# Performance work log

Hardware: AMD Instinct MI355X
Metric: run time of the kernel (lower is better)

The kernel has to match this reference:

```python
import jax, jax.numpy as jnp
import numpy as np

B, V, F, H, W = 8, 5023, 9976, 512, 512
L = 5  # lights


def setup_inputs() -> dict:
    key = jax.random.key(0)
    ks = jax.random.split(key, 7)
    return {
        "vertices": jax.random.normal(ks[0], (B, V, 3), jnp.float32),
        "transformed_vertices": jax.random.normal(ks[1], (B, V, 3), jnp.float32),
        "lights": jax.random.normal(ks[2], (B, L, 6), jnp.float32),
        "images": jax.random.uniform(ks[3], (B, 3, H, W), jnp.float32),
        "bary": jax.random.uniform(ks[4], (B, H, W, 3), jnp.float32) + 1e-3,
        "faces": jax.random.randint(ks[5], (F, 3), 0, V),
        "pix_to_face": jax.random.randint(ks[6], (B, H, W), 0, F + 1),  # ==F -> background
    }


def _face_vertices(verts, faces):
    # verts [B,V,3], faces [F,3] -> [B,F,3,3]  (gather)
    return verts[:, faces]


def _vertex_normals(verts, faces):
    # gather face verts, per-face cross products, scatter-add back to vertices
    fv = verts[:, faces]                       # [B,F,3,3]
    v0, v1, v2 = fv[:, :, 0], fv[:, :, 1], fv[:, :, 2]
    n = jnp.zeros_like(verts)
    n = n.at[:, faces[:, 1]].add(jnp.cross(v2 - v1, v0 - v1))
    n = n.at[:, faces[:, 2]].add(jnp.cross(v0 - v2, v1 - v2))
    n = n.at[:, faces[:, 0]].add(jnp.cross(v1 - v0, v2 - v0))
    return n / jnp.maximum(jnp.linalg.norm(n, axis=-1, keepdims=True), 1e-6)


def _add_directionlight(normals, lights):
    # normals [B,N,3], lights [B,L,6] -> shading [B,N,3]
    d = lights[:, :, :3]
    d = d / jnp.maximum(jnp.linalg.norm(d, axis=-1, keepdims=True), 1e-12)
    ndl = jnp.clip(jnp.einsum("bnc,blc->bln", normals, d), 0.0, 1.0)  # [B,L,N]
    return jnp.mean(ndl[..., None] * lights[:, :, None, 3:], axis=1)


def reference(vertices, transformed_vertices, lights, images, bary, faces, pix_to_face):
    sg = jax.lax.stop_gradient
    b, nv, _ = vertices.shape
    nf = faces.shape[0]
    h, w = pix_to_face.shape[1], pix_to_face.shape[2]

    tv = transformed_vertices.at[:, :, 2].add(10.0)

    fverts = _face_vertices(vertices, faces)                 # [B,F,3,3]
    normals = _vertex_normals(vertices, faces)               # [B,V,3]
    fnorm = _face_vertices(normals, faces)                   # [B,F,3,3]
    tnorm = _vertex_normals(tv, faces)
    tfnorm = _face_vertices(tnorm, faces)

    colors = jnp.full((b, nf, 3, 3), 180.0 / 255.0, vertices.dtype)  # face_colors buffer
    uv = jnp.zeros((b, nf, 3, 3), vertices.dtype)                    # face_uvcoords (unused downstream)
    # attribute channels: [0:3]=albedo [3:6]=tfnorm [6:9]=verts [9:12]=fnorm [12:15]=uv
    attrs = jnp.concatenate([colors, sg(tfnorm), sg(fverts), fnorm, uv], axis=-1)  # [B,F,3,15]

    # --- rasterizer interpolation stage ---
    p2f = pix_to_face.reshape(b, -1)                         # [B,HW]
    valid = (p2f < nf).astype(vertices.dtype)[..., None]     # [B,HW,1] alpha channel
    fidx = jnp.minimum(p2f, nf - 1)
    pa = jax.vmap(lambda a, i: a[i])(attrs, fidx)            # [B,HW,3,15]
    bw = bary.reshape(b, -1, 3)
    bw = bw / jnp.sum(bw, axis=-1, keepdims=True)
    interp = jnp.einsum("bpk,bpkc->bpc", bw, pa)             # [B,HW,15]

    albedo = interp[..., 0:3]
    tnormal_map = sg(interp[..., 3:6])
    pos_mask = (tnormal_map[..., 2:3] < 0.15).astype(vertices.dtype)
    normal_images = sg(interp[..., 9:12])
    alpha = sg(valid) * pos_mask                             # [B,HW,1]

    shading = _add_directionlight(normal_images, lights)     # [B,HW,3]
    shaded = albedo * shading

    imgs = images.transpose(0, 2, 3, 1).reshape(b, -1, 3)
    out = shaded * alpha + imgs * (1.0 - alpha)              # [B,HW,3]
    return out.reshape(b, h, w, 3).transpose(0, 3, 1, 2)     # [B,3,H,W]
```

## Files before the change

### kernel.cpp

```cpp
#include <hip/hip_runtime.h>
#include <stdint.h>

namespace {

constexpr int kB = 8;
constexpr int kV = 5023;
constexpr int kF = 9976;
constexpr int kH = 512;
constexpr int kW = 512;
constexpr int kL = 5;
constexpr int kHW = kH * kW;
constexpr int kQ = kHW / 4;
constexpr int kQH = kQ / 2;
constexpr int kCap = 32;

typedef float nfloat4 __attribute__((ext_vector_type(4)));

__device__ __forceinline__ float h2f(uint32_t u) {
  _Float16 h;
  uint16_t s = (uint16_t)u;
  __builtin_memcpy(&h, &s, 2);
  return (float)h;
}
__device__ __forceinline__ uint32_t f2h(float f) {
  _Float16 h = (_Float16)f;
  uint16_t s;
  __builtin_memcpy(&s, &h, 2);
  return (uint32_t)s;
}

__device__ __forceinline__ void cross3(float ax, float ay, float az,
                                       float bx, float by, float bz,
                                       float& cx, float& cy, float& cz) {
  cx = ay * bz - az * by;
  cy = az * bx - ax * bz;
  cz = ax * by - ay * bx;
}

__global__ void init_kernel(int* __restrict__ cnt,
                            const float* __restrict__ lights,
                            float4* __restrict__ ldir4) {
  int idx = blockIdx.x * blockDim.x + threadIdx.x;
  for (int i = idx; i < kV; i += gridDim.x * blockDim.x) cnt[i] = 0;
  if (idx < kB * kL) {
    float dx = lights[idx * 6 + 0];
    float dy = lights[idx * 6 + 1];
    float dz = lights[idx * 6 + 2];
    float inv = 1.0f / fmaxf(sqrtf(dx * dx + dy * dy + dz * dz), 1e-12f);
    ldir4[idx * 2 + 0] = make_float4(dx * inv, dy * inv, dz * inv, 0.0f);
    ldir4[idx * 2 + 1] =
        make_float4(lights[idx * 6 + 3], lights[idx * 6 + 4], lights[idx * 6 + 5], 0.0f);
  }
}

__global__ void prep_kernel(const float* __restrict__ verts,
                            const float* __restrict__ tverts,
                            const int* __restrict__ faces,
                            int* __restrict__ cnt,
                            int* __restrict__ adj,
                            float4* __restrict__ fn) {
  int idx = blockIdx.x * blockDim.x + threadIdx.x;
  if (idx < kF) {
    int f = idx;
#pragma unroll
    for (int c = 0; c < 3; ++c) {
      int v = faces[f * 3 + c];
      int slot = atomicAdd(&cnt[v], 1);
      if (slot < kCap) adj[v * kCap + slot] = f;
    }
    return;
  }
  idx -= kF;
  if (idx >= kB * kF) return;
  int b = idx / kF;
  int f = idx - b * kF;
  int i0 = faces[f * 3 + 0];
  int i1 = faces[f * 3 + 1];
  int i2 = faces[f * 3 + 2];

  float nx, ny, nz, tx, ty, tz;
  {
    const float* vb = verts + (size_t)b * kV * 3;
    float v0x = vb[i0 * 3 + 0], v0y = vb[i0 * 3 + 1], v0z = vb[i0 * 3 + 2];
    float v1x = vb[i1 * 3 + 0], v1y = vb[i1 * 3 + 1], v1z = vb[i1 * 3 + 2];
    float v2x = vb[i2 * 3 + 0], v2y = vb[i2 * 3 + 1], v2z = vb[i2 * 3 + 2];
    cross3(v1x - v0x, v1y - v0y, v1z - v0z, v2x - v0x, v2y - v0y, v2z - v0z,
           nx, ny, nz);
  }
  {
    const float* vb = tverts + (size_t)b * kV * 3;
    float v0x = vb[i0 * 3 + 0], v0y = vb[i0 * 3 + 1], v0z = vb[i0 * 3 + 2] + 10.0f;
    float v1x = vb[i1 * 3 + 0], v1y = vb[i1 * 3 + 1], v1z = vb[i1 * 3 + 2] + 10.0f;
    float v2x = vb[i2 * 3 + 0], v2y = vb[i2 * 3 + 1], v2z = vb[i2 * 3 + 2] + 10.0f;
    cross3(v1x - v0x, v1y - v0y, v1z - v0z, v2x - v0x, v2y - v0y, v2z - v0z,
           tx, ty, tz);
  }
  fn[(size_t)idx * 2 + 0] = make_float4(nx, ny, nz, tx);
  fn[(size_t)idx * 2 + 1] = make_float4(ty, tz, 0.0f, 0.0f);
}

__global__ void gather_normalize_kernel(const int* __restrict__ cnt,
                                        const int* __restrict__ adj,
                                        const float4* __restrict__ fn,
                                        uint4* __restrict__ vrec) {
  int idx = blockIdx.x * blockDim.x + threadIdx.x;
  if (idx >= kB * kV) return;
  int b = idx / kV;
  int v = idx - b * kV;
  int e = min(cnt[v], kCap);
  float nx = 0.f, ny = 0.f, nz = 0.f, tx = 0.f, ty = 0.f, tzv = 0.f;
  const int* av = adj + v * kCap;
  for (int j = 0; j < e; ++j) {
    int f = av[j];
    size_t k = ((size_t)b * kF + f) * 2;
    float4 a = fn[k];
    float4 c = fn[k + 1];
    nx += a.x;
    ny += a.y;
    nz += a.z;
    tx += a.w;
    ty += c.x;
    tzv += c.y;
  }
  float inv = 1.0f / fmaxf(sqrtf(nx * nx + ny * ny + nz * nz), 1e-6f);
  float invt = 1.0f / fmaxf(sqrtf(tx * tx + ty * ty + tzv * tzv), 1e-6f);
  uint4 r;
  r.x = f2h(nx * inv) | (f2h(ny * inv) << 16);
  r.y = f2h(nz * inv);
  r.z = __float_as_uint(tzv * invt);
  r.w = 0;
  vrec[idx] = r;
}

__global__ void faceattr_kernel(const int* __restrict__ faces,
                                const uint4* __restrict__ vrec,
                                uint4* __restrict__ fattr) {
  int b = blockIdx.x % kB;
  int f = (blockIdx.x / kB) * blockDim.x + threadIdx.x;
  if (f >= kF) return;
  int idx = b * kF + f;
  int i0 = faces[f * 3 + 0];
  int i1 = faces[f * 3 + 1];
  int i2 = faces[f * 3 + 2];
  const uint4* vb = vrec + (size_t)b * kV;
  uint4 r0 = vb[i0];
  uint4 r1 = vb[i1];
  uint4 r2 = vb[i2];
  uint4 w0, w1;
  w0.x = r0.x;
  w0.y = (r0.y & 0xffffu) | (r1.x << 16);
  w0.z = (r1.x >> 16) | ((r1.y & 0xffffu) << 16);
  w0.w = r2.x;
  w1.x = r2.y & 0xffffu;
  w1.y = r0.z;
  w1.z = r1.z;
  w1.w = r2.z;
  fattr[(size_t)idx * 2 + 0] = w0;
  fattr[(size_t)idx * 2 + 1] = w1;
}

__device__ __forceinline__ void shade_quad(
    const int4& f4, const float4& w0, const float4& w1, const float4& w2,
    const uint4* A, const uint4* T,
    const float4& im0, const float4& im1, const float4& im2,
    const float4* lb4, float o[3][4]) {
  int fi[4] = {f4.x, f4.y, f4.z, f4.w};
  float bw[4][3] = {{w0.x, w0.y, w0.z},
                    {w0.w, w1.x, w1.y},
                    {w1.z, w1.w, w2.x},
                    {w2.y, w2.z, w2.w}};
  float im[3][4] = {{im0.x, im0.y, im0.z, im0.w},
                    {im1.x, im1.y, im1.z, im1.w},
                    {im2.x, im2.y, im2.z, im2.w}};
#pragma unroll
  for (int k = 0; k < 4; ++k) {
    float b0 = bw[k][0], b1 = bw[k][1], b2 = bw[k][2];
    float inv = 1.0f / (b0 + b1 + b2);
    b0 *= inv;
    b1 *= inv;
    b2 *= inv;
    float n0x = h2f(A[k].x), n0y = h2f(A[k].x >> 16);
    float n0z = h2f(A[k].y), n1x = h2f(A[k].y >> 16);
    float n1y = h2f(A[k].z), n1z = h2f(A[k].z >> 16);
    float n2x = h2f(A[k].w), n2y = h2f(A[k].w >> 16);
    float n2z = h2f(T[k].x);
    float tz0 = __uint_as_float(T[k].y);
    float tz1 = __uint_as_float(T[k].z);
    float tz2 = __uint_as_float(T[k].w);

    float tzi = b0 * tz0 + b1 * tz1 + b2 * tz2;
    bool alpha = (fi[k] < kF) && (tzi < 0.15f);
    float nx = b0 * n0x + b1 * n1x + b2 * n2x;
    float ny = b0 * n0y + b1 * n1y + b2 * n2y;
    float nz = b0 * n0z + b1 * n1z + b2 * n2z;
    float s0 = 0.f, s1 = 0.f, s2 = 0.f;
#pragma unroll
    for (int l = 0; l < kL; ++l) {
      float4 d4 = lb4[l * 2 + 0];
      float4 c4 = lb4[l * 2 + 1];
      float d = nx * d4.x + ny * d4.y + nz * d4.z;
      d = fminf(fmaxf(d, 0.0f), 1.0f);
      s0 += d * c4.x;
      s1 += d * c4.y;
      s2 += d * c4.z;
    }
    const float kk = (180.0f / 255.0f) / (float)kL;
    o[0][k] = alpha ? kk * s0 : im[0][k];
    o[1][k] = alpha ? kk * s1 : im[1][k];
    o[2][k] = alpha ? kk * s2 : im[2][k];
  }
}

__global__ void __launch_bounds__(256) pixel8_kernel(
    const int4* __restrict__ p2f4,
    const float4* __restrict__ bary4,
    const uint4* __restrict__ fattr,
    const float4* __restrict__ ldir4,
    const float4* __restrict__ img4,
    float4* __restrict__ out4) {
  int b = blockIdx.x & 7;
  int q0 = (blockIdx.x >> 3) * blockDim.x + threadIdx.x;
  int q1 = q0 + kQH;
  size_t gA = (size_t)b * kQ + q0;
  size_t gB = (size_t)b * kQ + q1;

  int4 fA = p2f4[gA];
  int4 fB = p2f4[gB];
  float4 wA0 = bary4[gA * 3 + 0];
  float4 wA1 = bary4[gA * 3 + 1];
  float4 wA2 = bary4[gA * 3 + 2];
  float4 wB0 = bary4[gB * 3 + 0];
  float4 wB1 = bary4[gB * 3 + 1];
  float4 wB2 = bary4[gB * 3 + 2];

  size_t ibA = (size_t)b * 3 * kQ + q0;
  size_t ibB = (size_t)b * 3 * kQ + q1;
  float4 iA0 = img4[ibA + 0 * (size_t)kQ];
  float4 iA1 = img4[ibA + 1 * (size_t)kQ];
  float4 iA2 = img4[ibA + 2 * (size_t)kQ];
  float4 iB0 = img4[ibB + 0 * (size_t)kQ];
  float4 iB1 = img4[ibB + 1 * (size_t)kQ];
  float4 iB2 = img4[ibB + 2 * (size_t)kQ];

  uint4 AA[4], TA[4], AB[4], TB[4];
  {
    int fiA[4] = {fA.x, fA.y, fA.z, fA.w};
    int fiB[4] = {fB.x, fB.y, fB.z, fB.w};
#pragma unroll
    for (int k = 0; k < 4; ++k) {
      int f = (fiA[k] < kF) ? fiA[k] : (kF - 1);
      size_t base = ((size_t)b * kF + f) * 2;
      AA[k] = fattr[base + 0];
      TA[k] = fattr[base + 1];
    }
#pragma unroll
    for (int k = 0; k < 4; ++k) {
      int f = (fiB[k] < kF) ? fiB[k] : (kF - 1);
      size_t base = ((size_t)b * kF + f) * 2;
      AB[k] = fattr[base + 0];
      TB[k] = fattr[base + 1];
    }
  }

  int bu = __builtin_amdgcn_readfirstlane(b);
  const float4* lb4 = ldir4 + (size_t)bu * kL * 2;

  float oA[3][4];
  shade_quad(fA, wA0, wA1, wA2, AA, TA, iA0, iA1, iA2, lb4, oA);
#pragma unroll
  for (int c = 0; c < 3; ++c) {
    nfloat4 v = {oA[c][0], oA[c][1], oA[c][2], oA[c][3]};
    __builtin_nontemporal_store(v, (nfloat4*)&out4[ibA + c * (size_t)kQ]);
  }

  float oB[3][4];
  shade_quad(fB, wB0, wB1, wB2, AB, TB, iB0, iB1, iB2, lb4, oB);
#pragma unroll
  for (int c = 0; c < 3; ++c) {
    nfloat4 v = {oB[c][0], oB[c][1], oB[c][2], oB[c][3]};
    __builtin_nontemporal_store(v, (nfloat4*)&out4[ibB + c * (size_t)kQ]);
  }
}

}

extern "C" void kernel_launch(void* const* d_in, const int* in_sizes, int n_in,
                              void* d_out, int out_size, void* d_ws, size_t ws_size,
                              hipStream_t stream) {
  const float* vertices = (const float*)d_in[0];
  const float* tvertices = (const float*)d_in[1];
  const float* lights = (const float*)d_in[2];
  const float* images = (const float*)d_in[3];
  const float* bary = (const float*)d_in[4];
  const int* faces = (const int*)d_in[5];
  const int* p2f = (const int*)d_in[6];
  float* out = (float*)d_out;

  char* ws = (char*)d_ws;
  int* cnt = (int*)ws;
  ws += ((size_t)kV * sizeof(int) + 15) & ~15ull;
  int* adj = (int*)ws;
  ws += ((size_t)kV * kCap * sizeof(int) + 15) & ~15ull;
  float4* fn = (float4*)ws;
  ws += (size_t)kB * kF * 2 * sizeof(float4);
  uint4* vrec = (uint4*)ws;
  ws += (size_t)kB * kV * sizeof(uint4);
  float4* ldir4 = (float4*)ws;
  ws += (size_t)kB * kL * 2 * sizeof(float4);
  uint4* fattr = (uint4*)ws;

  {
    init_kernel<<<20, 256, 0, stream>>>(cnt, lights, ldir4);
  }
  {
    int n = kF + kB * kF;
    prep_kernel<<<(n + 255) / 256, 256, 0, stream>>>(vertices, tvertices, faces, cnt,
                                                     adj, fn);
  }
  {
    int n = kB * kV;
    gather_normalize_kernel<<<(n + 255) / 256, 256, 0, stream>>>(cnt, adj, fn, vrec);
  }
  {
    int chunks = (kF + 255) / 256;
    faceattr_kernel<<<chunks * kB, 256, 0, stream>>>(faces, vrec, fattr);
  }
  {
    pixel8_kernel<<<(kQH / 256) * kB, 256, 0, stream>>>(
        (const int4*)p2f, (const float4*)bary, fattr, ldir4, (const float4*)images,
        (float4*)out);
  }
}
```

Measured before the change: 47.02 us.

## Fuse four preprocessing kernels into one cooperative kernel with grid syncs

Merges the init, per-face normal, vertex gather-normalize and face-attribute kernels into one cooperative launch, with grid.sync() between the phases. The goal is to remove three kernel launches and their inter-kernel gaps. The grid is about 351 blocks of 256 threads, which must all be co-resident for a cooperative launch, and each grid-wide sync adds its own cost. Phase work is mapped directly by thread index, so every phase fits within this one grid.

Measured after the change: 161.6 us. 244% more time.

```diff
diff --git a/kernel.cpp b/kernel.cpp
--- a/kernel.cpp
+++ b/kernel.cpp
@@ -1,5 +1,8 @@
 #include <hip/hip_runtime.h>
+#include <hip/hip_cooperative_groups.h>
 #include <stdint.h>
+
+namespace cg = cooperative_groups;
 
 namespace {
 
@@ -14,6 +17,9 @@
 constexpr int kQH = kQ / 2;
 constexpr int kCap = 32;
 
+constexpr int kCoopThreads = kF + kB * kF;
+constexpr int kCoopBlocks = (kCoopThreads + 255) / 256;
+
 typedef float nfloat4 __attribute__((ext_vector_type(4)));
 
 __device__ __forceinline__ float h2f(uint32_t u) {
@@ -37,11 +43,21 @@
   cz = ax * by - ay * bx;
 }
 
-__global__ void init_kernel(int* __restrict__ cnt,
-                            const float* __restrict__ lights,
-                            float4* __restrict__ ldir4) {
-  int idx = blockIdx.x * blockDim.x + threadIdx.x;
-  for (int i = idx; i < kV; i += gridDim.x * blockDim.x) cnt[i] = 0;
+__global__ void fused_prep_kernel(const float* __restrict__ verts,
+                                  const float* __restrict__ tverts,
+                                  const int* __restrict__ faces,
+                                  const float* __restrict__ lights,
+                                  int* __restrict__ cnt,
+                                  int* __restrict__ adj,
+                                  float4* __restrict__ fn,
+                                  uint4* __restrict__ vrec,
+                                  uint4* __restrict__ fattr,
+                                  float4* __restrict__ ldir4) {
+  cg::grid_group grid = cg::this_grid();
+  const int idx = blockIdx.x * blockDim.x + threadIdx.x;
+  const int nthr = gridDim.x * blockDim.x;
+
+  for (int i = idx; i < kV; i += nthr) cnt[i] = 0;
   if (idx < kB * kL) {
     float dx = lights[idx * 6 + 0];
     float dy = lights[idx * 6 + 1];
@@ -51,15 +67,8 @@
     ldir4[idx * 2 + 1] =
         make_float4(lights[idx * 6 + 3], lights[idx * 6 + 4], lights[idx * 6 + 5], 0.0f);
   }
-}
-
-__global__ void prep_kernel(const float* __restrict__ verts,
-                            const float* __restrict__ tverts,
-                            const int* __restrict__ faces,
-                            int* __restrict__ cnt,
-                            int* __restrict__ adj,
-                            float4* __restrict__ fn) {
-  int idx = blockIdx.x * blockDim.x + threadIdx.x;
+  grid.sync();
+
   if (idx < kF) {
     int f = idx;
 #pragma unroll
@@ -68,95 +77,86 @@
       int slot = atomicAdd(&cnt[v], 1);
       if (slot < kCap) adj[v * kCap + slot] = f;
     }
-    return;
-  }
-  idx -= kF;
-  if (idx >= kB * kF) return;
-  int b = idx / kF;
-  int f = idx - b * kF;
-  int i0 = faces[f * 3 + 0];
-  int i1 = faces[f * 3 + 1];
-  int i2 = faces[f * 3 + 2];
-
-  float nx, ny, nz, tx, ty, tz;
-  {
-    const float* vb = verts + (size_t)b * kV * 3;
-    float v0x = vb[i0 * 3 + 0], v0y = vb[i0 * 3 + 1], v0z = vb[i0 * 3 + 2];
-    float v1x = vb[i1 * 3 + 0], v1y = vb[i1 * 3 + 1], v1z = vb[i1 * 3 + 2];
-    float v2x = vb[i2 * 3 + 0], v2y = vb[i2 * 3 + 1], v2z = vb[i2 * 3 + 2];
-    cross3(v1x - v0x, v1y - v0y, v1z - v0z, v2x - v0x, v2y - v0y, v2z - v0z,
-           nx, ny, nz);
-  }
-  {
-    const float* vb = tverts + (size_t)b * kV * 3;
-    float v0x = vb[i0 * 3 + 0], v0y = vb[i0 * 3 + 1], v0z = vb[i0 * 3 + 2] + 10.0f;
-    float v1x = vb[i1 * 3 + 0], v1y = vb[i1 * 3 + 1], v1z = vb[i1 * 3 + 2] + 10.0f;
-    float v2x = vb[i2 * 3 + 0], v2y = vb[i2 * 3 + 1], v2z = vb[i2 * 3 + 2] + 10.0f;
-    cross3(v1x - v0x, v1y - v0y, v1z - v0z, v2x - v0x, v2y - v0y, v2z - v0z,
-           tx, ty, tz);
-  }
-  fn[(size_t)idx * 2 + 0] = make_float4(nx, ny, nz, tx);
-  fn[(size_t)idx * 2 + 1] = make_float4(ty, tz, 0.0f, 0.0f);
-}
-
-__global__ void gather_normalize_kernel(const int* __restrict__ cnt,
-                                        const int* __restrict__ adj,
-                                        const float4* __restrict__ fn,
-                                        uint4* __restrict__ vrec) {
-  int idx = blockIdx.x * blockDim.x + threadIdx.x;
-  if (idx >= kB * kV) return;
-  int b = idx / kV;
-  int v = idx - b * kV;
-  int e = min(cnt[v], kCap);
-  float nx = 0.f, ny = 0.f, nz = 0.f, tx = 0.f, ty = 0.f, tzv = 0.f;
-  const int* av = adj + v * kCap;
-  for (int j = 0; j < e; ++j) {
-    int f = av[j];
-    size_t k = ((size_t)b * kF + f) * 2;
-    float4 a = fn[k];
-    float4 c = fn[k + 1];
-    nx += a.x;
-    ny += a.y;
-    nz += a.z;
-    tx += a.w;
-    ty += c.x;
-    tzv += c.y;
-  }
-  float inv = 1.0f / fmaxf(sqrtf(nx * nx + ny * ny + nz * nz), 1e-6f);
-  float invt = 1.0f / fmaxf(sqrtf(tx * tx + ty * ty + tzv * tzv), 1e-6f);
-  uint4 r;
-  r.x = f2h(nx * inv) | (f2h(ny * inv) << 16);
-  r.y = f2h(nz * inv);
-  r.z = __float_as_uint(tzv * invt);
-  r.w = 0;
-  vrec[idx] = r;
-}
-
-__global__ void faceattr_kernel(const int* __restrict__ faces,
-                                const uint4* __restrict__ vrec,
-                                uint4* __restrict__ fattr) {
-  int b = blockIdx.x % kB;
-  int f = (blockIdx.x / kB) * blockDim.x + threadIdx.x;
-  if (f >= kF) return;
-  int idx = b * kF + f;
-  int i0 = faces[f * 3 + 0];
-  int i1 = faces[f * 3 + 1];
-  int i2 = faces[f * 3 + 2];
-  const uint4* vb = vrec + (size_t)b * kV;
-  uint4 r0 = vb[i0];
-  uint4 r1 = vb[i1];
-  uint4 r2 = vb[i2];
-  uint4 w0, w1;
-  w0.x = r0.x;
-  w0.y = (r0.y & 0xffffu) | (r1.x << 16);
-  w0.z = (r1.x >> 16) | ((r1.y & 0xffffu) << 16);
-  w0.w = r2.x;
-  w1.x = r2.y & 0xffffu;
-  w1.y = r0.z;
-  w1.z = r1.z;
-  w1.w = r2.z;
-  fattr[(size_t)idx * 2 + 0] = w0;
-  fattr[(size_t)idx * 2 + 1] = w1;
+  } else if (idx < kF + kB * kF) {
+    int j = idx - kF;
+    int b = j / kF;
+    int f = j - b * kF;
+    int i0 = faces[f * 3 + 0];
+    int i1 = faces[f * 3 + 1];
+    int i2 = faces[f * 3 + 2];
+    float nx, ny, nz, tx, ty, tz;
+    {
+      const float* vb = verts + (size_t)b * kV * 3;
+      float v0x = vb[i0 * 3 + 0], v0y = vb[i0 * 3 + 1], v0z = vb[i0 * 3 + 2];
+      float v1x = vb[i1 * 3 + 0], v1y = vb[i1 * 3 + 1], v1z = vb[i1 * 3 + 2];
+      float v2x = vb[i2 * 3 + 0], v2y = vb[i2 * 3 + 1], v2z = vb[i2 * 3 + 2];
+      cross3(v1x - v0x, v1y - v0y, v1z - v0z, v2x - v0x, v2y - v0y, v2z - v0z,
+             nx, ny, nz);
+    }
+    {
+      const float* vb = tverts + (size_t)b * kV * 3;
+      float v0x = vb[i0 * 3 + 0], v0y = vb[i0 * 3 + 1], v0z = vb[i0 * 3 + 2] + 10.0f;
+      float v1x = vb[i1 * 3 + 0], v1y = vb[i1 * 3 + 1], v1z = vb[i1 * 3 + 2] + 10.0f;
+      float v2x = vb[i2 * 3 + 0], v2y = vb[i2 * 3 + 1], v2z = vb[i2 * 3 + 2] + 10.0f;
+      cross3(v1x - v0x, v1y - v0y, v1z - v0z, v2x - v0x, v2y - v0y, v2z - v0z,
+             tx, ty, tz);
+    }
+    fn[(size_t)j * 2 + 0] = make_float4(nx, ny, nz, tx);
+    fn[(size_t)j * 2 + 1] = make_float4(ty, tz, 0.0f, 0.0f);
+  }
+  grid.sync();
+
+  if (idx < kB * kV) {
+    int b = idx / kV;
+    int v = idx - b * kV;
+    int e = min(cnt[v], kCap);
+    float nx = 0.f, ny = 0.f, nz = 0.f, tx = 0.f, ty = 0.f, tzv = 0.f;
+    const int* av = adj + v * kCap;
+    for (int j = 0; j < e; ++j) {
+      int f = av[j];
+      size_t k = ((size_t)b * kF + f) * 2;
+      float4 a = fn[k];
+      float4 c = fn[k + 1];
+      nx += a.x;
+      ny += a.y;
+      nz += a.z;
+      tx += a.w;
+      ty += c.x;
+      tzv += c.y;
+    }
+    float inv = 1.0f / fmaxf(sqrtf(nx * nx + ny * ny + nz * nz), 1e-6f);
+    float invt = 1.0f / fmaxf(sqrtf(tx * tx + ty * ty + tzv * tzv), 1e-6f);
+    uint4 r;
+    r.x = f2h(nx * inv) | (f2h(ny * inv) << 16);
+    r.y = f2h(nz * inv);
+    r.z = __float_as_uint(tzv * invt);
+    r.w = 0;
+    vrec[idx] = r;
+  }
+  grid.sync();
+
+  if (idx < kB * kF) {
+    int b = idx / kF;
+    int f = idx - b * kF;
+    int i0 = faces[f * 3 + 0];
+    int i1 = faces[f * 3 + 1];
+    int i2 = faces[f * 3 + 2];
+    const uint4* vb = vrec + (size_t)b * kV;
+    uint4 r0 = vb[i0];
+    uint4 r1 = vb[i1];
+    uint4 r2 = vb[i2];
+    uint4 w0, w1;
+    w0.x = r0.x;
+    w0.y = (r0.y & 0xffffu) | (r1.x << 16);
+    w0.z = (r1.x >> 16) | ((r1.y & 0xffffu) << 16);
+    w0.w = r2.x;
+    w1.x = r2.y & 0xffffu;
+    w1.y = r0.z;
+    w1.z = r1.z;
+    w1.w = r2.z;
+    fattr[(size_t)idx * 2 + 0] = w0;
+    fattr[(size_t)idx * 2 + 1] = w1;
+  }
 }
 
 __device__ __forceinline__ void shade_quad(
@@ -310,20 +310,12 @@
   uint4* fattr = (uint4*)ws;
 
   {
-    init_kernel<<<20, 256, 0, stream>>>(cnt, lights, ldir4);
-  }
-  {
-    int n = kF + kB * kF;
-    prep_kernel<<<(n + 255) / 256, 256, 0, stream>>>(vertices, tvertices, faces, cnt,
-                                                     adj, fn);
-  }
-  {
-    int n = kB * kV;
-    gather_normalize_kernel<<<(n + 255) / 256, 256, 0, stream>>>(cnt, adj, fn, vrec);
-  }
-  {
-    int chunks = (kF + 255) / 256;
-    faceattr_kernel<<<chunks * kB, 256, 0, stream>>>(faces, vrec, fattr);
+    void* args[] = {(void*)&vertices, (void*)&tvertices, (void*)&faces,
+                    (void*)&lights,   (void*)&cnt,       (void*)&adj,
+                    (void*)&fn,       (void*)&vrec,      (void*)&fattr,
+                    (void*)&ldir4};
+    hipLaunchCooperativeKernel((const void*)fused_prep_kernel,
+                               dim3(kCoopBlocks), dim3(256), args, 0, stream);
   }
   {
     pixel8_kernel<<<(kQH / 256) * kB, 256, 0, stream>>>(
```
